# Performance work log

Measured on AMD Instinct MI355X. Metric: run time of the kernel, lower is better.

## Reference

```python
import jax, jax.numpy as jnp
from jax import lax
import numpy as np
import math

N_HEAD = 8
MAX_REL = 16


def _layer_norm(x, g, b, eps=1e-5):
    mu = jnp.mean(x, -1, keepdims=True)
    var = jnp.var(x, -1, keepdims=True)
    return (x - mu) / jnp.sqrt(var + eps) * g + b


def _pos_encoding(S, H):
    # PositionalEncoding buffer: row 0 is zeros, rows 1..para_limit are sin/cos of positions 0..para_limit-1
    pe = np.zeros((1001, H), np.float32)
    pos = np.arange(0, 1000, dtype=np.float32)[:, None]
    div = np.exp(np.arange(0, H, 2, dtype=np.float32) * (-math.log(10000.0) / H))
    pe[1:, 0::2] = np.sin(pos * div)
    pe[1:, 1::2] = np.cos(pos * div)
    return jnp.asarray(pe[:S])


def setup_inputs() -> dict:
    key = jax.random.key(0)
    B, S, H, NC, K = 32, 512, 512, 2, 7
    NH, M = N_HEAD, MAX_REL
    dk = H // NH
    V = 2 * M + 1
    ks = jax.random.split(key, 16)
    sd = 0.02
    f32 = jnp.float32
    return {
        "x": jax.random.normal(ks[0], (B, S, H), f32),
        "mask": jnp.ones((B, S), jnp.int32),
        # conv blocks (stacked over NC)
        "dw_w": (jax.random.normal(ks[1], (NC, H, 1, K), f32) * sd),
        "dw_b": jnp.zeros((NC, H), f32),
        "pw_w": (jax.random.normal(ks[2], (NC, H, H), f32) * sd),
        "pw_b": jnp.zeros((NC, H), f32),
        "ln_conv_g": jnp.ones((NC, H), f32),
        "ln_conv_b": jnp.zeros((NC, H), f32),
        # attention (torch Linear convention: W is (out,in))
        "wq": jax.random.normal(ks[3], (H, H), f32) * sd,
        "bq": jnp.zeros((H,), f32),
        "wk": jax.random.normal(ks[4], (H, H), f32) * sd,
        "bk": jnp.zeros((H,), f32),
        "wv": jax.random.normal(ks[5], (H, H), f32) * sd,
        "bv": jnp.zeros((H,), f32),
        "wo": jax.random.normal(ks[6], (H, H), f32) * sd,
        "bo": jnp.zeros((H,), f32),
        "embed_k": jax.random.normal(ks[7], (V, dk), f32) * sd,
        "embed_v": jax.random.normal(ks[8], (V, dk), f32) * sd,
        "ln_att_g": jnp.ones((H,), f32),
        "ln_att_b": jnp.zeros((H,), f32),
        # feed-forward block (hidden->hidden)
        "w_ff": jax.random.normal(ks[9], (H, H), f32) * sd,
        "b_ff": jnp.zeros((H,), f32),
        "ln_ffn_g": jnp.ones((H,), f32),
        "ln_ffn_b": jnp.zeros((H,), f32),
    }


def reference(x, mask, dw_w, dw_b, pw_w, pw_b, ln_conv_g, ln_conv_b,
              wq, bq, wk, bk, wv, bv, wo, bo, embed_k, embed_v,
              ln_att_g, ln_att_b, w_ff, b_ff, ln_ffn_g, ln_ffn_b):
    B, S, H = x.shape
    NH = N_HEAD
    dk = H // NH
    M = MAX_REL
    NC = dw_w.shape[0]
    K = dw_w.shape[-1]

    # positional encoding (scale_fact = 1)
    x = x + _pos_encoding(S, H)[None] * mask[..., None].astype(x.dtype)

    # conv blocks: x + relu(pointwise(depthwise(LN(x))))
    for i in range(NC):
        n = _layer_norm(x, ln_conv_g[i], ln_conv_b[i])
        h = n.transpose(0, 2, 1)  # (B,H,S)
        h = lax.conv_general_dilated(
            h, dw_w[i], window_strides=(1,), padding=[(K // 2, K // 2)],
            dimension_numbers=("NCH", "OIH", "NCH"), feature_group_count=H,
        ) + dw_b[i][None, :, None]
        h = jnp.einsum("bcs,oc->bos", h, pw_w[i]) + pw_b[i][None, :, None]
        h = jax.nn.relu(h).transpose(0, 2, 1)
        x = x + h

    # self-attention block with relative position representations (Shaw et al.)
    n = _layer_norm(x, ln_att_g, ln_att_b)
    q = (jnp.einsum("bsh,oh->bso", n, wq) + bq).reshape(B, S, NH, dk).transpose(0, 2, 1, 3)
    k = (jnp.einsum("bsh,oh->bso", n, wk) + bk).reshape(B, S, NH, dk).transpose(0, 2, 1, 3)
    v = (jnp.einsum("bsh,oh->bso", n, wv) + bv).reshape(B, S, NH, dk).transpose(0, 2, 1, 3)

    pos = jnp.arange(S)
    idx = jnp.clip(pos[None, :] - pos[:, None], -M, M) + M  # (S,S)
    rel_k = embed_k[idx]  # (S,S,dk)
    rel_v = embed_v[idx]  # (S,S,dk)

    # NOTE: original code applies no 1/sqrt(dk) scaling and effectively uses plain softmax
    logits = jnp.einsum("bhqd,bhkd->bhqk", q, k) + jnp.einsum("bhqd,qkd->bhqk", q, rel_k)
    w = jax.nn.softmax(logits, axis=-1)
    o = jnp.einsum("bhqk,bhkd->bhqd", w, v) + jnp.einsum("bhqk,qkd->bhqd", w, rel_v)
    o = o.transpose(0, 2, 1, 3).reshape(B, S, H)
    x = x + jnp.einsum("bsh,oh->bso", o, wo) + bo

    # feed-forward block: x + relu(Linear(LN(x)))
    n = _layer_norm(x, ln_ffn_g, ln_ffn_b)
    x = x + jax.nn.relu(jnp.einsum("bsh,oh->bso", n, w_ff) + b_ff)
    return x
```

## Files before the change

### kernel.cpp

```cpp
#include <hip/hip_runtime.h>

#define SEQ 512
#define HD 512
#define BATCH 32
#define TOK (BATCH * SEQ)
#define NHEAD 8
#define DKDIM 64
#define MREL 16
#define NRELV 33

using short8 = __attribute__((ext_vector_type(8))) short;
using f32x4  = __attribute__((ext_vector_type(4))) float;
using f32x16 = __attribute__((ext_vector_type(16))) float;
typedef unsigned short ushortT;

#define AS1 __attribute__((address_space(1)))
#define AS3 __attribute__((address_space(3)))
#define GLDS16(g, l) __builtin_amdgcn_global_load_lds( \
    (const AS1 unsigned int*)(const void*)(g), \
    (AS3 unsigned int*)(void*)(l), 16, 0, 0)

__device__ __forceinline__ ushortT f2bf(float x) {
  union { float f; unsigned u; } c; c.f = x;
  unsigned r = c.u + 0x7FFF + ((c.u >> 16) & 1);
  return (ushortT)(r >> 16);
}

__device__ __forceinline__ float bf2f(ushortT h) {
  union { unsigned u; float f; } c; c.u = (unsigned)h << 16;
  return c.f;
}

__global__ __launch_bounds__(256) void pe_kernel(float* __restrict__ PE) {
  const int i = blockIdx.x * 256 + threadIdx.x;
  const int s = i >> 9, h = i & (HD - 1);
  float v = 0.f;
  if (s > 0) {
    const int i2 = h & ~1;
    const float div = expf((float)i2 * (-9.210340371976184f / (float)HD));
    const float ang = (float)(s - 1) * div;
    v = (h & 1) ? cosf(ang) : sinf(ang);
  }
  PE[i] = v;
}

__global__ __launch_bounds__(256) void convw_kernel(
    const float* __restrict__ s0, const float* __restrict__ s1,
    const float* __restrict__ s2, const float* __restrict__ s3,
    const float* __restrict__ s4, const float* __restrict__ s5,
    const float* __restrict__ s6, ushortT* __restrict__ dst) {
  const int i = blockIdx.x * 256 + threadIdx.x;
  const int region = i >> 16;
  const int off = i & 65535;
  const float* s = region == 0 ? s0 : region == 1 ? s1 : region == 2 ? s2 :
                   region == 3 ? s3 : region == 4 ? s4 : region == 5 ? s5 : s6;
  const float4 v = ((const float4*)s)[off];
  ushort4 o;
  o.x = f2bf(v.x); o.y = f2bf(v.y); o.z = f2bf(v.z); o.w = f2bf(v.w);
  *(ushort4*)&dst[(long)i * 4] = o;
}

__global__ __launch_bounds__(256) void addpos_ln_kernel(
    const float* __restrict__ X, const int* __restrict__ mask,
    const float* __restrict__ PE, const float* __restrict__ g,
    const float* __restrict__ bta, float* __restrict__ out,
    ushortT* __restrict__ Y) {
  const int row = blockIdx.x;
  const int t = threadIdx.x;
  const int s0i = row & (SEQ - 1);
  const float mk = (float)mask[row];
  const float x0 = X[(long)row * HD + t]       + PE[s0i * HD + t] * mk;
  const float x1 = X[(long)row * HD + t + 256] + PE[s0i * HD + t + 256] * mk;
  out[(long)row * HD + t] = x0;
  out[(long)row * HD + t + 256] = x1;
  float s = x0 + x1, q = x0 * x0 + x1 * x1;
  #pragma unroll
  for (int off = 32; off > 0; off >>= 1) {
    s += __shfl_down(s, off);
    q += __shfl_down(q, off);
  }
  __shared__ float sh[10];
  const int w = t >> 6;
  if ((t & 63) == 0) { sh[w] = s; sh[4 + w] = q; }
  __syncthreads();
  if (t == 0) {
    const float S_ = sh[0] + sh[1] + sh[2] + sh[3];
    const float Q_ = sh[4] + sh[5] + sh[6] + sh[7];
    const float mu = S_ * (1.f / (float)HD);
    const float var = Q_ * (1.f / (float)HD) - mu * mu;
    sh[8] = mu;
    sh[9] = rsqrtf(var + 1e-5f);
  }
  __syncthreads();
  const float mu = sh[8], rstd = sh[9];
  ushortT* yr = Y + (long)row * HD;
  yr[t]       = f2bf((x0 - mu) * rstd * g[t] + bta[t]);
  yr[t + 256] = f2bf((x1 - mu) * rstd * g[t + 256] + bta[t + 256]);
}

template <bool BF>
__global__ __launch_bounds__(256) void ln_kernel(
    const float* __restrict__ X, const float* __restrict__ g,
    const float* __restrict__ bta, void* __restrict__ Yv) {
  const int row = blockIdx.x;
  const int t = threadIdx.x;
  const float* xr = X + (long)row * HD;
  const float x0 = xr[t], x1 = xr[t + 256];
  float s = x0 + x1, q = x0 * x0 + x1 * x1;
  #pragma unroll
  for (int off = 32; off > 0; off >>= 1) {
    s += __shfl_down(s, off);
    q += __shfl_down(q, off);
  }
  __shared__ float sh[10];
  const int w = t >> 6;
  if ((t & 63) == 0) { sh[w] = s; sh[4 + w] = q; }
  __syncthreads();
  if (t == 0) {
    const float S_ = sh[0] + sh[1] + sh[2] + sh[3];
    const float Q_ = sh[4] + sh[5] + sh[6] + sh[7];
    const float mu = S_ * (1.f / (float)HD);
    const float var = Q_ * (1.f / (float)HD) - mu * mu;
    sh[8] = mu;
    sh[9] = rsqrtf(var + 1e-5f);
  }
  __syncthreads();
  const float mu = sh[8], rstd = sh[9];
  const float y0 = (x0 - mu) * rstd * g[t] + bta[t];
  const float y1 = (x1 - mu) * rstd * g[t + 256] + bta[t + 256];
  if (BF) {
    ushortT* yr = (ushortT*)Yv + (long)row * HD;
    yr[t] = f2bf(y0);
    yr[t + 256] = f2bf(y1);
  } else {
    float* yr = (float*)Yv + (long)row * HD;
    yr[t] = y0;
    yr[t + 256] = y1;
  }
}

__global__ __launch_bounds__(256) void dwconv_kernel(
    const ushortT* __restrict__ N_, const float* __restrict__ w,
    const float* __restrict__ bias, ushortT* __restrict__ Hout) {
  const int t = threadIdx.x;
  const int cg = t & 63, sb = t >> 6;
  const int tile = blockIdx.x;
  const int b = tile >> 5;
  const int s0 = ((tile & 31) << 4) + (sb << 2);
  const long rowb = (long)b * SEQ;
  const int c0 = cg * 8;

  float wr[56];
  #pragma unroll
  for (int i = 0; i < 14; ++i) {
    const float4 v = *(const float4*)&w[c0 * 7 + i * 4];
    wr[i * 4 + 0] = v.x; wr[i * 4 + 1] = v.y;
    wr[i * 4 + 2] = v.z; wr[i * 4 + 3] = v.w;
  }
  float bz[8];
  #pragma unroll
  for (int i = 0; i < 2; ++i) {
    const float4 v = *(const float4*)&bias[c0 + i * 4];
    bz[i * 4 + 0] = v.x; bz[i * 4 + 1] = v.y;
    bz[i * 4 + 2] = v.z; bz[i * 4 + 3] = v.w;
  }

  const short8 zero = {};
  short8 win[7];
  #pragma unroll
  for (int k = 0; k < 7; ++k) {
    const int ss = s0 + k - 3;
    win[k] = (ss >= 0 && ss < SEQ) ? *(const short8*)&N_[(rowb + ss) * HD + c0] : zero;
  }
  #pragma unroll
  for (int u = 0; u < 4; ++u) {
    float acc[8];
    #pragma unroll
    for (int j = 0; j < 8; ++j) acc[j] = bz[j];
    #pragma unroll
    for (int k = 0; k < 7; ++k)
      #pragma unroll
      for (int j = 0; j < 8; ++j)
        acc[j] += bf2f((ushortT)win[k][j]) * wr[j * 7 + k];
    short8 o;
    #pragma unroll
    for (int j = 0; j < 8; ++j) o[j] = (short)f2bf(acc[j]);
    *(short8*)&Hout[(rowb + s0 + u) * HD + c0] = o;
    if (u < 3) {
      #pragma unroll
      for (int k = 0; k < 6; ++k) win[k] = win[k + 1];
      const int ss = s0 + u + 4;
      win[6] = (ss < SEQ) ? *(const short8*)&N_[(rowb + ss) * HD + c0] : zero;
    }
  }
}

__device__ __forceinline__ void gemm_tile(
    const ushortT* __restrict__ A, const ushortT* __restrict__ W,
    int row0, int col0, int t, ushortT* Als, ushortT* Bls, f32x4 acc[4][4]) {
  const int lane = t & 63, w = t >> 6;
  const int wr = w >> 1, wc = w & 1;
  const int l15 = lane & 15, lhi = lane >> 4;
  for (int kt = 0; kt < 8; ++kt) {
    __syncthreads();
    #pragma unroll
    for (int i = 0; i < 4; ++i) {
      const int tl = i * 256 + t;
      const int r = tl >> 3, sl = tl & 7;
      const int sc = sl ^ (r & 7);
      GLDS16(A + (long)(row0 + r) * HD + kt * 64 + sc * 8,
             Als + (i * 256 + w * 64) * 8);
      GLDS16(W + (long)(col0 + r) * HD + kt * 64 + sc * 8,
             Bls + (i * 256 + w * 64) * 8);
    }
    __syncthreads();
    #pragma unroll
    for (int kk = 0; kk < 2; ++kk) {
      short8 af[4], bf[4];
      #pragma unroll
      for (int i = 0; i < 4; ++i) {
        const int ra = wr * 64 + i * 16 + l15;
        const int rb = wc * 64 + i * 16 + l15;
        af[i] = *(const short8*)&Als[ra * 64 + (((kk * 4 + lhi) ^ (ra & 7)) << 3)];
        bf[i] = *(const short8*)&Bls[rb * 64 + (((kk * 4 + lhi) ^ (rb & 7)) << 3)];
      }
      #pragma unroll
      for (int mi = 0; mi < 4; ++mi)
        #pragma unroll
        for (int ni = 0; ni < 4; ++ni)
          acc[mi][ni] = __builtin_amdgcn_mfma_f32_16x16x32_bf16(af[mi], bf[ni], acc[mi][ni], 0, 0, 0);
    }
  }
}

template <int MODE>
__global__ __launch_bounds__(512) void mgemm512_kernel(
    const ushortT* __restrict__ A, const ushortT* __restrict__ W,
    const float* __restrict__ bias, float* __restrict__ C,
    ushortT* __restrict__ Cb) {
  __shared__ ushortT Als[128 * 64];
  __shared__ ushortT Bls[128 * 64];
  const int t = threadIdx.x;
  const int bid = blockIdx.x;
  const int m_blk = (bid & 7) * 16 + ((bid >> 3) & 15);
  const int n_blk = bid >> 7;
  const int row0 = m_blk * 128, col0 = n_blk * 128;
  const int lane = t & 63, w = t >> 6;
  const int wr = w >> 2, wc = w & 3;
  const int l15 = lane & 15, lhi = lane >> 4;

  f32x4 acc[4][2] = {};

  for (int kt = 0; kt < 8; ++kt) {
    __syncthreads();
    #pragma unroll
    for (int i = 0; i < 2; ++i) {
      const int tl = i * 512 + t;
      const int r = tl >> 3, sl = tl & 7;
      const int sc = sl ^ (r & 7);
      GLDS16(A + (long)(row0 + r) * HD + kt * 64 + sc * 8,
             Als + (i * 512 + w * 64) * 8);
      GLDS16(W + (long)(col0 + r) * HD + kt * 64 + sc * 8,
             Bls + (i * 512 + w * 64) * 8);
    }
    __syncthreads();
    #pragma unroll
    for (int kk = 0; kk < 2; ++kk) {
      short8 af[4], bf[2];
      #pragma unroll
      for (int i = 0; i < 4; ++i) {
        const int ra = wr * 64 + i * 16 + l15;
        af[i] = *(const short8*)&Als[ra * 64 + (((kk * 4 + lhi) ^ (ra & 7)) << 3)];
      }
      #pragma unroll
      for (int j = 0; j < 2; ++j) {
        const int rb = wc * 32 + j * 16 + l15;
        bf[j] = *(const short8*)&Bls[rb * 64 + (((kk * 4 + lhi) ^ (rb & 7)) << 3)];
      }
      #pragma unroll
      for (int mi = 0; mi < 4; ++mi)
        #pragma unroll
        for (int ni = 0; ni < 2; ++ni)
          acc[mi][ni] = __builtin_amdgcn_mfma_f32_16x16x32_bf16(af[mi], bf[ni], acc[mi][ni], 0, 0, 0);
    }
  }

  #pragma unroll
  for (int ni = 0; ni < 2; ++ni) {
    const int c = col0 + wc * 32 + ni * 16 + l15;
    const float bz = bias[c];
    #pragma unroll
    for (int mi = 0; mi < 4; ++mi) {
      #pragma unroll
      for (int reg = 0; reg < 4; ++reg) {
        const int rrow = row0 + wr * 64 + mi * 16 + lhi * 4 + reg;
        const float g = acc[mi][ni][reg] + bz;
        const long idx = (long)rrow * HD + c;
        if (MODE == 0)      C[idx] = g;
        else if (MODE == 1) C[idx] += g;
        else if (MODE == 2) C[idx] += fmaxf(g, 0.f);
        else                Cb[idx] = f2bf(g);
      }
    }
  }
}

__global__ __launch_bounds__(256) void qkv_kernel(
    const ushortT* __restrict__ A, const ushortT* __restrict__ Wbase,
    const float* __restrict__ bq, const float* __restrict__ bk,
    const float* __restrict__ bv, ushortT* __restrict__ Q,
    ushortT* __restrict__ K, ushortT* __restrict__ Vt) {
  __shared__ ushortT Als[128 * 64];
  __shared__ ushortT Bls[128 * 64];
  const int t = threadIdx.x;
  const int z = blockIdx.y;
  const ushortT* W = Wbase + (long)z * HD * HD;
  const float* bias = z == 0 ? bq : z == 1 ? bk : bv;
  const int bid = blockIdx.x;
  const int m_blk = (bid & 7) * 16 + ((bid >> 3) & 15);
  const int n_blk = bid >> 7;
  const int row0 = m_blk * 128, col0 = n_blk * 128;
  const int lane = t & 63, w = t >> 6;
  const int wr = w >> 1, wc = w & 1;
  const int l15 = lane & 15, lhi = lane >> 4;

  f32x4 acc[4][4] = {};
  gemm_tile(A, W, row0, col0, t, Als, Bls, acc);

  #pragma unroll
  for (int ni = 0; ni < 4; ++ni) {
    const int c = col0 + wc * 64 + ni * 16 + l15;
    const float bz = bias[c];
    #pragma unroll
    for (int mi = 0; mi < 4; ++mi) {
      if (z == 2) {
        const int tok0 = row0 + wr * 64 + mi * 16 + lhi * 4;
        const int b = tok0 >> 9, s = tok0 & (SEQ - 1);
        const int h = c >> 6, d = c & 63;
        ushort4 pk;
        pk.x = f2bf(acc[mi][ni][0] + bz);
        pk.y = f2bf(acc[mi][ni][1] + bz);
        pk.z = f2bf(acc[mi][ni][2] + bz);
        pk.w = f2bf(acc[mi][ni][3] + bz);
        *(ushort4*)&Vt[((long)((b * NHEAD + h) * DKDIM + d) << 9) + s] = pk;
      } else {
        ushortT* Cb = (z == 0) ? Q : K;
        #pragma unroll
        for (int reg = 0; reg < 4; ++reg) {
          const int rrow = row0 + wr * 64 + mi * 16 + lhi * 4 + reg;
          Cb[(long)rrow * HD + c] = f2bf(acc[mi][ni][reg] + bz);
        }
      }
    }
  }
}

__global__ __launch_bounds__(512, 4) void attn_kernel(
    const ushortT* __restrict__ Qg, const ushortT* __restrict__ Kg,
    const ushortT* __restrict__ Vt, const float* __restrict__ ekg,
    const float* __restrict__ evg, ushortT* __restrict__ Og) {
  __shared__ ushortT qekL[8][32][34];
  __shared__ ushortT wsAll[8][32][56];
  __shared__ ushortT EVT[64][56];
  __shared__ float LROWw[8][32];
  __shared__ float WHIw[8][32];

  const int t = threadIdx.x;
  const int lane = t & 63, w = t >> 6;
  const int l31 = lane & 31, h = lane >> 5;
  const int hh = blockIdx.x, qb = blockIdx.y, bb = blockIdx.z;
  const int q0w = qb * 256 + w * 32;
  const long qkb = ((long)bb * SEQ) * HD + hh * DKDIM;
  const long vtb = (long)(bb * NHEAD + hh) * DKDIM * SEQ;

  for (int i = t; i < 64 * 56; i += 512) {
    const int d = i / 56, r = i % 56;
    EVT[d][r] = (r < NRELV) ? f2bf(evg[r * 64 + d]) : (ushortT)0;
  }
  {
    unsigned* wz = (unsigned*)&wsAll[w][0][0];
    #pragma unroll
    for (int i = 0; i < 14; ++i) wz[lane + i * 64] = 0u;
  }
  __syncthreads();

  short8 qB[4];
  #pragma unroll
  for (int kk = 0; kk < 4; ++kk)
    qB[kk] = *(const short8*)&Qg[qkb + (long)(q0w + l31) * HD + kk * 16 + h * 8];

  {
    f32x16 qacc = {};
    #pragma unroll
    for (int kk = 0; kk < 4; ++kk) {
      short8 ef;
      #pragma unroll
      for (int j = 0; j < 8; ++j)
        ef[j] = (short)f2bf(ekg[l31 * 64 + kk * 16 + h * 8 + j]);
      qacc = __builtin_amdgcn_mfma_f32_32x32x16_bf16(ef, qB[kk], qacc, 0, 0, 0);
    }
    #pragma unroll
    for (int r = 0; r < 16; ++r) {
      const int rr = (r & 3) + 8 * (r >> 2) + 4 * h;
      qekL[w][l31][rr] = f2bf(qacc[r]);
    }
  }
  float qekHiR = 0.f, qekLoR = 0.f;
  #pragma unroll
  for (int kk = 0; kk < 4; ++kk)
    #pragma unroll
    for (int j = 0; j < 8; ++j) {
      const float qv = bf2f((ushortT)qB[kk][j]);
      const int d = kk * 16 + h * 8 + j;
      qekHiR += qv * ekg[32 * 64 + d];
      qekLoR += qv * ekg[d];
    }
  qekHiR += __shfl_xor(qekHiR, 32);
  qekLoR += __shfl_xor(qekLoR, 32);
  if (h == 0) qekL[w][l31][32] = f2bf(qekHiR);

  const int qg = q0w + l31;
  f32x16 oaccL = {}, oaccH = {};
  float rsum = 0.f, wsHi = 0.f;

  short8 kf[4];
  #pragma unroll
  for (int kk = 0; kk < 4; ++kk)
    kf[kk] = *(const short8*)&Kg[qkb + (long)l31 * HD + kk * 16 + h * 8];

  for (int kt = 0; kt < 16; ++kt) {
    const int k0 = kt * 32;
    short8 vf[4];
    vf[0] = *(const short8*)&Vt[vtb + (long)l31 * SEQ + k0 + h * 8];
    vf[1] = *(const short8*)&Vt[vtb + (long)(32 + l31) * SEQ + k0 + h * 8];
    vf[2] = *(const short8*)&Vt[vtb + (long)l31 * SEQ + k0 + 16 + h * 8];
    vf[3] = *(const short8*)&Vt[vtb + (long)(32 + l31) * SEQ + k0 + 16 + h * 8];

    f32x16 sacc = {};
    __builtin_amdgcn_s_setprio(1);
    #pragma unroll
    for (int kk = 0; kk < 4; ++kk)
      sacc = __builtin_amdgcn_mfma_f32_32x32x16_bf16(kf[kk], qB[kk], sacc, 0, 0, 0);
    __builtin_amdgcn_s_setprio(0);

    const int kn = (kt < 15) ? (k0 + 32) : k0;
    short8 kfn[4];
    #pragma unroll
    for (int kk = 0; kk < 4; ++kk)
      kfn[kk] = *(const short8*)&Kg[qkb + (long)(kn + l31) * HD + kk * 16 + h * 8];

    const int dmin = k0 - q0w - 31, dmax = k0 + 31 - q0w;
    if (dmin >= MREL) {
      #pragma unroll
      for (int r = 0; r < 16; ++r) {
        const float p = __expf(sacc[r] + qekHiR);
        sacc[r] = p; rsum += p; wsHi += p;
      }
    } else if (dmax <= -MREL) {
      #pragma unroll
      for (int r = 0; r < 16; ++r) {
        const float p = __expf(sacc[r] + qekLoR);
        sacc[r] = p; rsum += p;
      }
    } else {
      #pragma unroll
      for (int r = 0; r < 16; ++r) {
        const int key = k0 + (r & 3) + 8 * (r >> 2) + 4 * h;
        const int db = key - qg;
        const int rcl = min(max(db, -MREL), MREL) + MREL;
        const float p = __expf(sacc[r] + bf2f(qekL[w][l31][rcl]));
        sacc[r] = p; rsum += p;
        if (db >= MREL)       wsHi += p;
        else if (db > -MREL)  wsAll[w][l31][db + MREL] = f2bf(p);
      }
    }
    #pragma unroll
    for (int c = 0; c < 2; ++c) {
      const int rb = c * 8;
      unsigned a0, a1, b0, b1;
      asm("v_cvt_pk_bf16_f32 %0, %1, %2" : "=v"(a0) : "v"(sacc[rb + 0]), "v"(sacc[rb + 1]));
      asm("v_cvt_pk_bf16_f32 %0, %1, %2" : "=v"(a1) : "v"(sacc[rb + 2]), "v"(sacc[rb + 3]));
      asm("v_cvt_pk_bf16_f32 %0, %1, %2" : "=v"(b0) : "v"(sacc[rb + 4]), "v"(sacc[rb + 5]));
      asm("v_cvt_pk_bf16_f32 %0, %1, %2" : "=v"(b1) : "v"(sacc[rb + 6]), "v"(sacc[rb + 7]));
      asm("v_permlane32_swap_b32 %0, %1" : "+v"(a0), "+v"(b0));
      asm("v_permlane32_swap_b32 %0, %1" : "+v"(a1), "+v"(b1));
      union { unsigned u[4]; short8 s; } pa;
      pa.u[0] = a0; pa.u[1] = a1; pa.u[2] = b0; pa.u[3] = b1;
      __builtin_amdgcn_s_setprio(1);
      oaccL = __builtin_amdgcn_mfma_f32_32x32x16_bf16(pa.s, vf[c * 2 + 0], oaccL, 0, 0, 0);
      oaccH = __builtin_amdgcn_mfma_f32_32x32x16_bf16(pa.s, vf[c * 2 + 1], oaccH, 0, 0, 0);
      __builtin_amdgcn_s_setprio(0);
    }
    #pragma unroll
    for (int kk = 0; kk < 4; ++kk) kf[kk] = kfn[kk];
  }

  rsum += __shfl_xor(rsum, 32);
  wsHi += __shfl_xor(wsHi, 32);
  if (h == 0) { LROWw[w][l31] = rsum; WHIw[w][l31] = wsHi; }

  if (h == 0) {
    float ms = 0.f;
    #pragma unroll
    for (int cch = 0; cch < 4; ++cch) {
      const short8 v = *(const short8*)&wsAll[w][l31][cch * 8];
      #pragma unroll
      for (int j = 0; j < 8; ++j) ms += bf2f((ushortT)v[j]);
    }
    wsAll[w][l31][0]  = f2bf(rsum - wsHi - ms);
    wsAll[w][l31][32] = f2bf(wsHi);
  }

  #pragma unroll
  for (int kk = 0; kk < 3; ++kk) {
    const short8 aw = *(const short8*)&wsAll[w][l31][kk * 16 + h * 8];
    const short8 bL = *(const short8*)&EVT[l31][kk * 16 + h * 8];
    const short8 bH = *(const short8*)&EVT[l31 + 32][kk * 16 + h * 8];
    oaccL = __builtin_amdgcn_mfma_f32_32x32x16_bf16(aw, bL, oaccL, 0, 0, 0);
    oaccH = __builtin_amdgcn_mfma_f32_32x32x16_bf16(aw, bH, oaccH, 0, 0, 0);
  }

  const int dl = l31;
  #pragma unroll
  for (int r = 0; r < 16; ++r) {
    const int qr = (r & 3) + 8 * (r >> 2) + 4 * h;
    const float rinv = 1.f / LROWw[w][qr];
    const long orow = qkb + (long)(q0w + qr) * HD;
    Og[orow + dl] = f2bf(oaccL[r] * rinv);
    Og[orow + dl + 32] = f2bf(oaccH[r] * rinv);
  }
}

extern "C" void kernel_launch(void* const* d_in, const int* in_sizes, int n_in,
                              void* d_out, int out_size, void* d_ws, size_t ws_size,
                              hipStream_t stream) {
  const float* x    = (const float*)d_in[0];
  const int*   mask = (const int*)d_in[1];
  const float* dw_w = (const float*)d_in[2];
  const float* dw_b = (const float*)d_in[3];
  const float* pw_w = (const float*)d_in[4];
  const float* pw_b = (const float*)d_in[5];
  const float* lncg = (const float*)d_in[6];
  const float* lncb = (const float*)d_in[7];
  const float* wq   = (const float*)d_in[8];
  const float* bq   = (const float*)d_in[9];
  const float* wk   = (const float*)d_in[10];
  const float* bk   = (const float*)d_in[11];
  const float* wv   = (const float*)d_in[12];
  const float* bv   = (const float*)d_in[13];
  const float* wo   = (const float*)d_in[14];
  const float* bo   = (const float*)d_in[15];
  const float* ek   = (const float*)d_in[16];
  const float* ev   = (const float*)d_in[17];
  const float* lnag = (const float*)d_in[18];
  const float* lnab = (const float*)d_in[19];
  const float* wff  = (const float*)d_in[20];
  const float* bff  = (const float*)d_in[21];
  const float* lnfg = (const float*)d_in[22];
  const float* lnfb = (const float*)d_in[23];

  float* out = (float*)d_out;
  float* PE   = (float*)d_ws;
  float* NB32 = PE + SEQ * HD;
  ushortT* ABF = (ushortT*)(NB32 + (long)TOK * HD);
  ushortT* QBF = ABF + (long)TOK * HD;
  ushortT* KBF = QBF + (long)TOK * HD;
  ushortT* VTB = KBF + (long)TOK * HD;
  ushortT* WBF = VTB + (long)TOK * HD;
  const long WSZ = (long)HD * HD;

  pe_kernel<<<SEQ * HD / 256, 256, 0, stream>>>(PE);
  convw_kernel<<<7 * HD * HD / 4 / 256, 256, 0, stream>>>(
      pw_w, pw_w + WSZ, wq, wk, wv, wo, wff, WBF);
  addpos_ln_kernel<<<TOK, 256, 0, stream>>>(x, mask, PE, lncg, lncb, out, QBF);

  dwconv_kernel<<<BATCH * SEQ / 16, 256, 0, stream>>>(QBF, dw_w, dw_b, ABF);
  mgemm512_kernel<2><<<512, 512, 0, stream>>>(ABF, WBF, pw_b, out, nullptr);

  ln_kernel<true><<<TOK, 256, 0, stream>>>(out, lncg + HD, lncb + HD, QBF);
  dwconv_kernel<<<BATCH * SEQ / 16, 256, 0, stream>>>(QBF, dw_w + HD * 7, dw_b + HD, ABF);
  mgemm512_kernel<2><<<512, 512, 0, stream>>>(ABF, WBF + WSZ, pw_b + HD, out, nullptr);

  ln_kernel<true><<<TOK, 256, 0, stream>>>(out, lnag, lnab, ABF);
  qkv_kernel<<<dim3(512, 3), 256, 0, stream>>>(ABF, WBF + 2 * WSZ, bq, bk, bv, QBF, KBF, VTB);
  attn_kernel<<<dim3(NHEAD, SEQ / 256, BATCH), 512, 0, stream>>>(QBF, KBF, VTB, ek, ev, ABF);
  mgemm512_kernel<1><<<512, 512, 0, stream>>>(ABF, WBF + 5 * WSZ, bo, out, nullptr);

  ln_kernel<true><<<TOK, 256, 0, stream>>>(out, lnfg, lnfb, ABF);
  mgemm512_kernel<2><<<512, 512, 0, stream>>>(ABF, WBF + 6 * WSZ, bff, out, nullptr);
}
```

Baseline: 283.3 us.

## Store Q/K/V in MFMA-fragment-contiguous layout and load fragments directly

The QKV projection epilogue now writes Q, K and V into a per-(batch, head) tiled layout. Each 32-row by 8-element MFMA fragment becomes a contiguous 256-element block, so every wave's short8 loads in the attention kernel coalesce fully instead of striding by HD or SEQ. The attention loop also drops the explicit next-tile K prefetch and the hoisted V loads, issuing the loads just before their MFMAs. This gains coalescing but risks exposing load latency that the software prefetch used to hide, and the projection's Q/K stores become scattered 2-byte writes.

```diff
diff --git a/kernel.cpp b/kernel.cpp
--- a/kernel.cpp
+++ b/kernel.cpp
@@ -335,20 +335,28 @@
     for (int mi = 0; mi < 4; ++mi) {
       if (z == 2) {
         const int tok0 = row0 + wr * 64 + mi * 16 + lhi * 4;
-        const int b = tok0 >> 9, s = tok0 & (SEQ - 1);
-        const int h = c >> 6, d = c & 63;
+        const int b = tok0 >> 9, s0 = tok0 & (SEQ - 1);
+        const int hh2 = c >> 6, dd = c & 63;
         ushort4 pk;
         pk.x = f2bf(acc[mi][ni][0] + bz);
         pk.y = f2bf(acc[mi][ni][1] + bz);
         pk.z = f2bf(acc[mi][ni][2] + bz);
         pk.w = f2bf(acc[mi][ni][3] + bz);
-        *(ushort4*)&Vt[((long)((b * NHEAD + h) * DKDIM + d) << 9) + s] = pk;
+        const long off = ((((long)(b * NHEAD + hh2) * 16 + (s0 >> 5)) * 4 +
+                           ((s0 & 31) >> 3)) * 2 + (dd >> 5)) * 256 +
+                         (dd & 31) * 8 + (s0 & 7);
+        *(ushort4*)&Vt[off] = pk;
       } else {
         ushortT* Cb = (z == 0) ? Q : K;
+        const int hh2 = c >> 6, dd = c & 63;
         #pragma unroll
         for (int reg = 0; reg < 4; ++reg) {
           const int rrow = row0 + wr * 64 + mi * 16 + lhi * 4 + reg;
-          Cb[(long)rrow * HD + c] = f2bf(acc[mi][ni][reg] + bz);
+          const int b = rrow >> 9, s = rrow & (SEQ - 1);
+          const long off = ((((long)(b * NHEAD + hh2) * 16 + (s >> 5)) * 4 +
+                             (dd >> 4)) * 2 + ((dd >> 3) & 1)) * 256 +
+                           (s & 31) * 8 + (dd & 7);
+          Cb[off] = f2bf(acc[mi][ni][reg] + bz);
         }
       }
     }
@@ -356,8 +364,8 @@
 }
 
 __global__ __launch_bounds__(512, 4) void attn_kernel(
-    const ushortT* __restrict__ Qg, const ushortT* __restrict__ Kg,
-    const ushortT* __restrict__ Vt, const float* __restrict__ ekg,
+    const ushortT* __restrict__ Qf, const ushortT* __restrict__ Kf,
+    const ushortT* __restrict__ Vf, const float* __restrict__ ekg,
     const float* __restrict__ evg, ushortT* __restrict__ Og) {
   __shared__ ushortT qekL[8][32][34];
   __shared__ ushortT wsAll[8][32][56];
@@ -371,7 +379,7 @@
   const int hh = blockIdx.x, qb = blockIdx.y, bb = blockIdx.z;
   const int q0w = qb * 256 + w * 32;
   const long qkb = ((long)bb * SEQ) * HD + hh * DKDIM;
-  const long vtb = (long)(bb * NHEAD + hh) * DKDIM * SEQ;
+  const long fbase = (long)(bb * NHEAD + hh) * 16;
 
   for (int i = t; i < 64 * 56; i += 512) {
     const int d = i / 56, r = i % 56;
@@ -387,7 +395,7 @@
   short8 qB[4];
   #pragma unroll
   for (int kk = 0; kk < 4; ++kk)
-    qB[kk] = *(const short8*)&Qg[qkb + (long)(q0w + l31) * HD + kk * 16 + h * 8];
+    qB[kk] = *(const short8*)&Qf[(((fbase + qb * 8 + w) * 4 + kk) * 2 + h) * 256 + l31 * 8];
 
   {
     f32x16 qacc = {};
@@ -423,32 +431,16 @@
   f32x16 oaccL = {}, oaccH = {};
   float rsum = 0.f, wsHi = 0.f;
 
-  short8 kf[4];
-  #pragma unroll
-  for (int kk = 0; kk < 4; ++kk)
-    kf[kk] = *(const short8*)&Kg[qkb + (long)l31 * HD + kk * 16 + h * 8];
-
   for (int kt = 0; kt < 16; ++kt) {
     const int k0 = kt * 32;
-    short8 vf[4];
-    vf[0] = *(const short8*)&Vt[vtb + (long)l31 * SEQ + k0 + h * 8];
-    vf[1] = *(const short8*)&Vt[vtb + (long)(32 + l31) * SEQ + k0 + h * 8];
-    vf[2] = *(const short8*)&Vt[vtb + (long)l31 * SEQ + k0 + 16 + h * 8];
-    vf[3] = *(const short8*)&Vt[vtb + (long)(32 + l31) * SEQ + k0 + 16 + h * 8];
-
     f32x16 sacc = {};
     __builtin_amdgcn_s_setprio(1);
     #pragma unroll
-    for (int kk = 0; kk < 4; ++kk)
-      sacc = __builtin_amdgcn_mfma_f32_32x32x16_bf16(kf[kk], qB[kk], sacc, 0, 0, 0);
+    for (int kk = 0; kk < 4; ++kk) {
+      const short8 kf = *(const short8*)&Kf[(((fbase + kt) * 4 + kk) * 2 + h) * 256 + l31 * 8];
+      sacc = __builtin_amdgcn_mfma_f32_32x32x16_bf16(kf, qB[kk], sacc, 0, 0, 0);
+    }
     __builtin_amdgcn_s_setprio(0);
-
-    const int kn = (kt < 15) ? (k0 + 32) : k0;
-    short8 kfn[4];
-    #pragma unroll
-    for (int kk = 0; kk < 4; ++kk)
-      kfn[kk] = *(const short8*)&Kg[qkb + (long)(kn + l31) * HD + kk * 16 + h * 8];
-
     const int dmin = k0 - q0w - 31, dmax = k0 + 31 - q0w;
     if (dmin >= MREL) {
       #pragma unroll
@@ -486,13 +478,13 @@
       asm("v_permlane32_swap_b32 %0, %1" : "+v"(a1), "+v"(b1));
       union { unsigned u[4]; short8 s; } pa;
       pa.u[0] = a0; pa.u[1] = a1; pa.u[2] = b0; pa.u[3] = b1;
+      const short8 v0 = *(const short8*)&Vf[((((fbase + kt) * 4 + c * 2 + h) * 2 + 0) * 256) + l31 * 8];
+      const short8 v1 = *(const short8*)&Vf[((((fbase + kt) * 4 + c * 2 + h) * 2 + 1) * 256) + l31 * 8];
       __builtin_amdgcn_s_setprio(1);
-      oaccL = __builtin_amdgcn_mfma_f32_32x32x16_bf16(pa.s, vf[c * 2 + 0], oaccL, 0, 0, 0);
-      oaccH = __builtin_amdgcn_mfma_f32_32x32x16_bf16(pa.s, vf[c * 2 + 1], oaccH, 0, 0, 0);
+      oaccL = __builtin_amdgcn_mfma_f32_32x32x16_bf16(pa.s, v0, oaccL, 0, 0, 0);
+      oaccH = __builtin_amdgcn_mfma_f32_32x32x16_bf16(pa.s, v1, oaccH, 0, 0, 0);
       __builtin_amdgcn_s_setprio(0);
     }
-    #pragma unroll
-    for (int kk = 0; kk < 4; ++kk) kf[kk] = kfn[kk];
   }
 
   rsum += __shfl_xor(rsum, 32);
```

New measurement: 253.8 us. 1.12x faster.
